# Optimization experiments

Measured on AMD Instinct MI355X. Metric: run time of the kernel, lower is better.

## Reference

```python
import jax, jax.numpy as jnp
from jax import lax
import numpy as np

B, T, V = 2048, 128, 25
H = 512          # num_hidden
NUM_CLASSES = 100


def setup_inputs() -> dict:
    key = jax.random.key(0)
    ks = jax.random.split(key, 7)
    messages = jax.random.normal(ks[0], (B, T, V), dtype=jnp.float32)
    # LSTMCell params (PyTorch layout: weight_ih [4H, V], weight_hh [4H, H], gate order i,f,g,o)
    W_ih = jax.random.normal(ks[1], (4 * H, V), dtype=jnp.float32) * (1.0 / np.sqrt(V))
    W_hh = jax.random.normal(ks[2], (4 * H, H), dtype=jnp.float32) * (1.0 / np.sqrt(H))
    b_ih = jnp.zeros((4 * H,), dtype=jnp.float32)
    # forget-gate bias initialized to 1 (as in initialize_parameters)
    b_hh = jnp.zeros((4 * H,), dtype=jnp.float32).at[H:2 * H].set(1.0)
    W_fc = jax.random.normal(ks[3], (NUM_CLASSES, H), dtype=jnp.float32) * (1.0 / np.sqrt(H))
    b_fc = jnp.zeros((NUM_CLASSES,), dtype=jnp.float32)
    return {"messages": messages, "W_ih": W_ih, "W_hh": W_hh,
            "b_ih": b_ih, "b_hh": b_hh, "W_fc": W_fc, "b_fc": b_fc}


def reference(messages, W_ih, W_hh, b_ih, b_hh, W_fc, b_fc):
    b, t, v = messages.shape
    h_dim = W_hh.shape[1]
    # Batch the input-to-hidden projection across all timesteps up front: [B,T,4H]
    x_proj = jnp.einsum('btv,gv->btg', messages, W_ih) + b_ih + b_hh
    xs = jnp.swapaxes(x_proj, 0, 1)  # [T, B, 4H] for scan over time

    def step(carry, x_g):
        h, c = carry
        gates = x_g + h @ W_hh.T                       # [B, 4H]
        i, f, g, o = jnp.split(gates, 4, axis=-1)      # PyTorch gate order i,f,g,o
        i = jax.nn.sigmoid(i)
        f = jax.nn.sigmoid(f)
        g = jnp.tanh(g)
        o = jax.nn.sigmoid(o)
        c = f * c + i * g
        h = o * jnp.tanh(c)
        return (h, c), None

    init = (jnp.zeros((b, h_dim), dtype=messages.dtype),
            jnp.zeros((b, h_dim), dtype=messages.dtype))
    (h_last, _), _ = lax.scan(step, init, xs)
    return h_last @ W_fc.T + b_fc  # [B, num_classes]
```

## Files before the change

kernel.cpp:

```cpp
#include <hip/hip_runtime.h>

#define BB 2048
#define TT 128
#define VV 25
#define HH 512
#define NC 100

typedef __attribute__((ext_vector_type(8))) _Float16 half8;
typedef __attribute__((ext_vector_type(4))) float f32x4;

__device__ __forceinline__ float fsigmoid(float x) { return 1.0f / (1.0f + __expf(-x)); }
__device__ __forceinline__ float ftanh(float x) {
    float e = __expf(2.0f * x);
    return 1.0f - 2.0f / (e + 1.0f);
}

__global__ __launch_bounds__(256) void prep_whh_t(const float* __restrict__ W,
                                                  _Float16* __restrict__ WT) {
    int i = blockIdx.x * 256 + threadIdx.x;
    int n = i & 2047, kq = i >> 11;
    half8 h8;
    #pragma unroll
    for (int j = 0; j < 8; ++j) h8[j] = (_Float16)W[(size_t)n * HH + kq * 8 + j];
    ((half8*)WT)[(size_t)kq * 2048 + n] = h8;
}

__global__ __launch_bounds__(256) void prep_wih_t(const float* __restrict__ W,
                                                  _Float16* __restrict__ WT) {
    int i = blockIdx.x * 256 + threadIdx.x;
    int n = i & 2047, kq4 = i >> 11;
    half8 h8;
    #pragma unroll
    for (int j = 0; j < 8; ++j) {
        int k = kq4 * 8 + j;
        h8[j] = (k < VV) ? (_Float16)W[(size_t)n * VV + k] : (_Float16)0.0f;
    }
    ((half8*)WT)[(size_t)(64 + kq4) * 2048 + n] = h8;
}

__global__ __launch_bounds__(256, 2) void lstm_step(
    const float* __restrict__ msg, int t,
    const _Float16* __restrict__ WT,
    const float* __restrict__ b_ih, const float* __restrict__ b_hh,
    const _Float16* __restrict__ hin, _Float16* __restrict__ hout,
    float* __restrict__ c)
{
    const int b0 = blockIdx.x * 64;
    const int j0 = blockIdx.y * 32;
    const int tid = threadIdx.x;
    const int lane = tid & 63;
    const int w = tid >> 6;
    const int wm = w & 1, wn = w >> 1;
    const int col = lane & 15, quad = lane >> 4;
    const int jj = j0 + wn * 16 + col;

    __shared__ _Float16 Abuf[2][64][72];

    f32x4 acc[2][4];
    #pragma unroll
    for (int g = 0; g < 4; ++g) {
        float bias = b_ih[g * HH + jj] + b_hh[g * HH + jj];
        f32x4 bv = {bias, bias, bias, bias};
        acc[0][g] = bv;
        acc[1][g] = bv;
    }

    const int arow = tid >> 2, aseg = (tid & 3) << 4;
    const _Float16* aph = hin + (size_t)(b0 + arow) * HH + aseg;

    const half8* WT8 = (const half8*)WT;
    int bidx[4];
    #pragma unroll
    for (int g = 0; g < 4; ++g) bidx[g] = quad * 2048 + g * HH + j0 + wn * 16 + col;

    half8 Bs[2][4];
    half8 ra[2];

    ra[0] = *(const half8*)(aph);
    ra[1] = *(const half8*)(aph + 8);
    #pragma unroll
    for (int g = 0; g < 4; ++g) Bs[0][g] = WT8[bidx[g]];
    *(half8*)&Abuf[0][arow][aseg]     = ra[0];
    *(half8*)&Abuf[0][arow][aseg + 8] = ra[1];
    ra[0] = *(const half8*)(aph + 64);
    ra[1] = *(const half8*)(aph + 72);
    #pragma unroll
    for (int g = 0; g < 4; ++g) Bs[1][g] = WT8[8192 + bidx[g]];
    __syncthreads();

    float xv[8];
    const int xseg = (tid & 3) << 3;

    for (int it = 0; it < 8; ++it) {
        const int buf = it & 1;
        #pragma unroll
        for (int kk = 0; kk < 2; ++kk) {
            const int cchunk = it * 2 + kk;
            const int p = cchunk & 1;
            half8 ahf[2];
            #pragma unroll
            for (int tm = 0; tm < 2; ++tm)
                ahf[tm] = *(const half8*)&Abuf[buf][wm * 32 + tm * 16 + col][kk * 32 + quad * 8];
            #pragma unroll
            for (int tm = 0; tm < 2; ++tm)
                #pragma unroll
                for (int g = 0; g < 4; ++g)
                    acc[tm][g] = __builtin_amdgcn_mfma_f32_16x16x32_f16(ahf[tm], Bs[p][g], acc[tm][g], 0, 0, 0);
            if (cchunk + 2 <= 16) {
                const int ix = (cchunk + 2) * 8192;
                #pragma unroll
                for (int g = 0; g < 4; ++g) Bs[p][g] = WT8[ix + bidx[g]];
            }
        }
        if (it < 7) {
            *(half8*)&Abuf[buf ^ 1][arow][aseg]     = ra[0];
            *(half8*)&Abuf[buf ^ 1][arow][aseg + 8] = ra[1];
            if (it < 6) {
                const int kt = (it + 2) * 64;
                ra[0] = *(const half8*)(aph + kt);
                ra[1] = *(const half8*)(aph + kt + 8);
            } else {
                const size_t mb = ((size_t)(b0 + arow) * TT + t) * VV;
                #pragma unroll
                for (int i = 0; i < 8; ++i) {
                    int k = xseg + i;
                    xv[i] = (k < VV) ? msg[mb + k] : 0.0f;
                }
            }
        } else {
            half8 xh;
            #pragma unroll
            for (int i = 0; i < 8; ++i) xh[i] = (_Float16)xv[i];
            *(half8*)&Abuf[0][arow][xseg] = xh;
        }
        __syncthreads();
    }

    {
        half8 ahf[2];
        #pragma unroll
        for (int tm = 0; tm < 2; ++tm)
            ahf[tm] = *(const half8*)&Abuf[0][wm * 32 + tm * 16 + col][quad * 8];
        #pragma unroll
        for (int tm = 0; tm < 2; ++tm)
            #pragma unroll
            for (int g = 0; g < 4; ++g)
                acc[tm][g] = __builtin_amdgcn_mfma_f32_16x16x32_f16(ahf[tm], Bs[0][g], acc[tm][g], 0, 0, 0);
    }

    #pragma unroll
    for (int tm = 0; tm < 2; ++tm) {
        #pragma unroll
        for (int reg = 0; reg < 4; ++reg) {
            int b = b0 + wm * 32 + tm * 16 + quad * 4 + reg;
            size_t idx = (size_t)b * HH + jj;
            float i_ = fsigmoid(acc[tm][0][reg]);
            float f_ = fsigmoid(acc[tm][1][reg]);
            float g_ = ftanh(acc[tm][2][reg]);
            float o_ = fsigmoid(acc[tm][3][reg]);
            float cn = f_ * c[idx] + i_ * g_;
            c[idx] = cn;
            hout[idx] = (_Float16)(o_ * ftanh(cn));
        }
    }
}

__global__ __launch_bounds__(256) void fc_kernel(
    const _Float16* __restrict__ h, const float* __restrict__ W_fc,
    const float* __restrict__ b_fc, float* __restrict__ out)
{
    __shared__ float hs[4][HH];
    const int b0 = blockIdx.x * 4;
    for (int i = threadIdx.x; i < 4 * HH; i += 256) {
        int r = i >> 9, k = i & 511;
        hs[r][k] = (float)h[(size_t)(b0 + r) * HH + k];
    }
    __syncthreads();
    const int tid = threadIdx.x;
    if (tid < 2 * NC) {
        int r = tid / NC, cls = tid % NC;
        const float4* wv = (const float4*)(W_fc + (size_t)cls * HH);
        const float4* h0 = (const float4*)hs[r];
        const float4* h1 = (const float4*)hs[r + 2];
        float s0 = 0.0f, s1 = 0.0f;
        #pragma unroll 4
        for (int k = 0; k < HH / 4; ++k) {
            float4 ww = wv[k];
            float4 a0 = h0[k], a1 = h1[k];
            s0 += a0.x * ww.x + a0.y * ww.y + a0.z * ww.z + a0.w * ww.w;
            s1 += a1.x * ww.x + a1.y * ww.y + a1.z * ww.z + a1.w * ww.w;
        }
        out[(size_t)(b0 + r) * NC + cls] = s0 + b_fc[cls];
        out[(size_t)(b0 + r + 2) * NC + cls] = s1 + b_fc[cls];
    }
}

extern "C" void kernel_launch(void* const* d_in, const int* in_sizes, int n_in,
                              void* d_out, int out_size, void* d_ws, size_t ws_size,
                              hipStream_t stream) {
    const float* msg  = (const float*)d_in[0];
    const float* W_ih = (const float*)d_in[1];
    const float* W_hh = (const float*)d_in[2];
    const float* b_ih = (const float*)d_in[3];
    const float* b_hh = (const float*)d_in[4];
    const float* W_fc = (const float*)d_in[5];
    const float* b_fc = (const float*)d_in[6];
    float* out = (float*)d_out;

    float*    c  = (float*)d_ws;
    _Float16* h0 = (_Float16*)(c + (size_t)BB * HH);
    _Float16* h1 = h0 + (size_t)BB * HH;
    _Float16* WT = h1 + (size_t)BB * HH;

    hipMemsetAsync(d_ws, 0, (size_t)BB * HH * 4 + (size_t)BB * HH * 2, stream);

    prep_whh_t<<<512, 256, 0, stream>>>(W_hh, WT);
    prep_wih_t<<<32, 256, 0, stream>>>(W_ih, WT);

    _Float16 *hin = h0, *hout = h1;
    for (int t = 0; t < TT; ++t) {
        lstm_step<<<dim3(BB / 64, HH / 32), 256, 0, stream>>>(
            msg, t, WT, b_ih, b_hh, hin, hout, c);
        _Float16* tmp = hin; hin = hout; hout = tmp;
    }
    fc_kernel<<<BB / 4, 256, 0, stream>>>(hin, W_fc, b_fc, out);
}
```

Before: 1.558 ms.

## Load LSTM hidden-state operands directly into registers, drop LDS staging and memset

Replaces the shared-memory double-buffered staging of h with direct per-lane global loads into MFMA operand registers, using a 4-deep register prefetch ring for both A and B fragments and removing all __syncthreads. The t=0 step skips the recurrent matmul and the c read, so the workspace memset goes away. This removes LDS traffic and barrier stalls, but each lane now loads its own h rows with less coalesced access, and register pressure rises, which could hurt occupancy.

```diff
diff --git a/kernel.cpp b/kernel.cpp
--- a/kernel.cpp
+++ b/kernel.cpp
@@ -53,8 +53,7 @@
     const int wm = w & 1, wn = w >> 1;
     const int col = lane & 15, quad = lane >> 4;
     const int jj = j0 + wn * 16 + col;
-
-    __shared__ _Float16 Abuf[2][64][72];
+    const bool first = (t == 0);
 
     f32x4 acc[2][4];
     #pragma unroll
@@ -65,87 +64,90 @@
         acc[1][g] = bv;
     }
 
-    const int arow = tid >> 2, aseg = (tid & 3) << 4;
-    const _Float16* aph = hin + (size_t)(b0 + arow) * HH + aseg;
-
     const half8* WT8 = (const half8*)WT;
     int bidx[4];
     #pragma unroll
-    for (int g = 0; g < 4; ++g) bidx[g] = quad * 2048 + g * HH + j0 + wn * 16 + col;
-
-    half8 Bs[2][4];
-    half8 ra[2];
-
-    ra[0] = *(const half8*)(aph);
-    ra[1] = *(const half8*)(aph + 8);
-    #pragma unroll
-    for (int g = 0; g < 4; ++g) Bs[0][g] = WT8[bidx[g]];
-    *(half8*)&Abuf[0][arow][aseg]     = ra[0];
-    *(half8*)&Abuf[0][arow][aseg + 8] = ra[1];
-    ra[0] = *(const half8*)(aph + 64);
-    ra[1] = *(const half8*)(aph + 72);
-    #pragma unroll
-    for (int g = 0; g < 4; ++g) Bs[1][g] = WT8[8192 + bidx[g]];
-    __syncthreads();
-
-    float xv[8];
-    const int xseg = (tid & 3) << 3;
-
-    for (int it = 0; it < 8; ++it) {
-        const int buf = it & 1;
-        #pragma unroll
-        for (int kk = 0; kk < 2; ++kk) {
-            const int cchunk = it * 2 + kk;
-            const int p = cchunk & 1;
-            half8 ahf[2];
+    for (int g = 0; g < 4; ++g) bidx[g] = quad * 2048 + g * HH + jj;
+
+    const _Float16* aB[2];
+    #pragma unroll
+    for (int tm = 0; tm < 2; ++tm)
+        aB[tm] = hin + (size_t)(b0 + wm * 32 + tm * 16 + col) * HH + quad * 8;
+
+    float xv[2][8];
+    #pragma unroll
+    for (int tm = 0; tm < 2; ++tm) {
+        const size_t mb = ((size_t)(b0 + wm * 32 + tm * 16 + col) * TT + t) * VV;
+        #pragma unroll
+        for (int j = 0; j < 8; ++j) {
+            int k = quad * 8 + j;
+            xv[tm][j] = (k < VV) ? msg[mb + k] : 0.0f;
+        }
+    }
+
+    half8 Ah[4][2];
+    half8 Bs[4][4];
+
+    if (!first) {
+        #pragma unroll
+        for (int pc = 0; pc < 4; ++pc) {
             #pragma unroll
             for (int tm = 0; tm < 2; ++tm)
-                ahf[tm] = *(const half8*)&Abuf[buf][wm * 32 + tm * 16 + col][kk * 32 + quad * 8];
+                Ah[pc][tm] = *(const half8*)(aB[tm] + pc * 32);
+            #pragma unroll
+            for (int g = 0; g < 4; ++g)
+                Bs[pc][g] = WT8[pc * 8192 + bidx[g]];
+        }
+        #pragma unroll
+        for (int cc = 0; cc < 16; ++cc) {
+            const int sl = cc & 3;
             #pragma unroll
             for (int tm = 0; tm < 2; ++tm)
                 #pragma unroll
                 for (int g = 0; g < 4; ++g)
-                    acc[tm][g] = __builtin_amdgcn_mfma_f32_16x16x32_f16(ahf[tm], Bs[p][g], acc[tm][g], 0, 0, 0);
-            if (cchunk + 2 <= 16) {
-                const int ix = (cchunk + 2) * 8192;
-                #pragma unroll
-                for (int g = 0; g < 4; ++g) Bs[p][g] = WT8[ix + bidx[g]];
+                    acc[tm][g] = __builtin_amdgcn_mfma_f32_16x16x32_f16(Ah[sl][tm], Bs[sl][g], acc[tm][g], 0, 0, 0);
+            const int pf = cc + 4;
+            if (pf < 16) {
+                #pragma unroll
+                for (int tm = 0; tm < 2; ++tm)
+                    Ah[sl][tm] = *(const half8*)(aB[tm] + pf * 32);
+                #pragma unroll
+                for (int g = 0; g < 4; ++g)
+                    Bs[sl][g] = WT8[pf * 8192 + bidx[g]];
+            } else if (pf == 16) {
+                #pragma unroll
+                for (int tm = 0; tm < 2; ++tm) {
+                    half8 xh;
+                    #pragma unroll
+                    for (int j = 0; j < 8; ++j) xh[j] = (_Float16)xv[tm][j];
+                    Ah[sl][tm] = xh;
+                }
+                #pragma unroll
+                for (int g = 0; g < 4; ++g)
+                    Bs[sl][g] = WT8[16 * 8192 + bidx[g]];
             }
         }
-        if (it < 7) {
-            *(half8*)&Abuf[buf ^ 1][arow][aseg]     = ra[0];
-            *(half8*)&Abuf[buf ^ 1][arow][aseg + 8] = ra[1];
-            if (it < 6) {
-                const int kt = (it + 2) * 64;
-                ra[0] = *(const half8*)(aph + kt);
-                ra[1] = *(const half8*)(aph + kt + 8);
-            } else {
-                const size_t mb = ((size_t)(b0 + arow) * TT + t) * VV;
-                #pragma unroll
-                for (int i = 0; i < 8; ++i) {
-                    int k = xseg + i;
-                    xv[i] = (k < VV) ? msg[mb + k] : 0.0f;
-                }
-            }
-        } else {
+        #pragma unroll
+        for (int tm = 0; tm < 2; ++tm)
+            #pragma unroll
+            for (int g = 0; g < 4; ++g)
+                acc[tm][g] = __builtin_amdgcn_mfma_f32_16x16x32_f16(Ah[0][tm], Bs[0][g], acc[tm][g], 0, 0, 0);
+    } else {
+        #pragma unroll
+        for (int tm = 0; tm < 2; ++tm) {
             half8 xh;
             #pragma unroll
-            for (int i = 0; i < 8; ++i) xh[i] = (_Float16)xv[i];
-            *(half8*)&Abuf[0][arow][xseg] = xh;
-        }
-        __syncthreads();
-    }
-
-    {
-        half8 ahf[2];
+            for (int j = 0; j < 8; ++j) xh[j] = (_Float16)xv[tm][j];
+            Ah[0][tm] = xh;
+        }
+        #pragma unroll
+        for (int g = 0; g < 4; ++g)
+            Bs[0][g] = WT8[16 * 8192 + bidx[g]];
         #pragma unroll
         for (int tm = 0; tm < 2; ++tm)
-            ahf[tm] = *(const half8*)&Abuf[0][wm * 32 + tm * 16 + col][quad * 8];
-        #pragma unroll
-        for (int tm = 0; tm < 2; ++tm)
             #pragma unroll
             for (int g = 0; g < 4; ++g)
-                acc[tm][g] = __builtin_amdgcn_mfma_f32_16x16x32_f16(ahf[tm], Bs[0][g], acc[tm][g], 0, 0, 0);
+                acc[tm][g] = __builtin_amdgcn_mfma_f32_16x16x32_f16(Ah[0][tm], Bs[0][g], acc[tm][g], 0, 0, 0);
     }
 
     #pragma unroll
@@ -158,7 +160,8 @@
             float f_ = fsigmoid(acc[tm][1][reg]);
             float g_ = ftanh(acc[tm][2][reg]);
             float o_ = fsigmoid(acc[tm][3][reg]);
-            float cn = f_ * c[idx] + i_ * g_;
+            float cn = i_ * g_;
+            if (!first) cn = __builtin_fmaf(f_, c[idx], cn);
             c[idx] = cn;
             hout[idx] = (_Float16)(o_ * ftanh(cn));
         }
@@ -212,8 +215,6 @@
     _Float16* h1 = h0 + (size_t)BB * HH;
     _Float16* WT = h1 + (size_t)BB * HH;
 
-    hipMemsetAsync(d_ws, 0, (size_t)BB * HH * 4 + (size_t)BB * HH * 2, stream);
-
     prep_whh_t<<<512, 256, 0, stream>>>(W_hh, WT);
     prep_wih_t<<<32, 256, 0, stream>>>(W_ih, WT);
 
```

New measurement: 2.690 ms. 1.73x slower.

## Deepen weight prefetch, skip h-GEMM at t=0, load x directly into registers

Applied to the files above, without the earlier changes.

The weight-fragment register pipeline grows from two to four chunks, so global loads of W have more MFMA work to hide behind. Barriers now wait only on LDS counters rather than draining global loads. The message input is loaded straight into MFMA A-fragment registers instead of going through LDS. At t=0 the recurrent GEMM and the c read are skipped because h and c are zero, which also removes the workspace memset. The deeper prefetch raises register pressure, which may lower occupancy under the 2-blocks-per-SM launch bound.

```diff
diff --git a/kernel.cpp b/kernel.cpp
--- a/kernel.cpp
+++ b/kernel.cpp
@@ -13,6 +13,13 @@
 __device__ __forceinline__ float ftanh(float x) {
     float e = __expf(2.0f * x);
     return 1.0f - 2.0f / (e + 1.0f);
+}
+
+__device__ __forceinline__ void bar_nodrain() {
+    asm volatile("s_waitcnt lgkmcnt(0)" ::: "memory");
+    __builtin_amdgcn_sched_barrier(0);
+    __builtin_amdgcn_s_barrier();
+    asm volatile("" ::: "memory");
 }
 
 __global__ __launch_bounds__(256) void prep_whh_t(const float* __restrict__ W,
@@ -53,6 +60,7 @@
     const int wm = w & 1, wn = w >> 1;
     const int col = lane & 15, quad = lane >> 4;
     const int jj = j0 + wn * 16 + col;
+    const bool first = (t == 0);
 
     __shared__ _Float16 Abuf[2][64][72];
 
@@ -71,76 +79,102 @@
     const half8* WT8 = (const half8*)WT;
     int bidx[4];
     #pragma unroll
-    for (int g = 0; g < 4; ++g) bidx[g] = quad * 2048 + g * HH + j0 + wn * 16 + col;
-
-    half8 Bs[2][4];
+    for (int g = 0; g < 4; ++g) bidx[g] = quad * 2048 + g * HH + jj;
+
+    half8 Bs[4][4];
     half8 ra[2];
-
-    ra[0] = *(const half8*)(aph);
-    ra[1] = *(const half8*)(aph + 8);
-    #pragma unroll
-    for (int g = 0; g < 4; ++g) Bs[0][g] = WT8[bidx[g]];
-    *(half8*)&Abuf[0][arow][aseg]     = ra[0];
-    *(half8*)&Abuf[0][arow][aseg + 8] = ra[1];
-    ra[0] = *(const half8*)(aph + 64);
-    ra[1] = *(const half8*)(aph + 72);
-    #pragma unroll
-    for (int g = 0; g < 4; ++g) Bs[1][g] = WT8[8192 + bidx[g]];
-    __syncthreads();
-
-    float xv[8];
-    const int xseg = (tid & 3) << 3;
-
-    for (int it = 0; it < 8; ++it) {
-        const int buf = it & 1;
-        #pragma unroll
-        for (int kk = 0; kk < 2; ++kk) {
-            const int cchunk = it * 2 + kk;
-            const int p = cchunk & 1;
-            half8 ahf[2];
-            #pragma unroll
-            for (int tm = 0; tm < 2; ++tm)
-                ahf[tm] = *(const half8*)&Abuf[buf][wm * 32 + tm * 16 + col][kk * 32 + quad * 8];
-            #pragma unroll
-            for (int tm = 0; tm < 2; ++tm)
+    float xv[2][8];
+
+    if (!first) {
+        ra[0] = *(const half8*)(aph);
+        ra[1] = *(const half8*)(aph + 8);
+        #pragma unroll
+        for (int pc = 0; pc < 4; ++pc)
+            #pragma unroll
+            for (int g = 0; g < 4; ++g) Bs[pc][g] = WT8[pc * 8192 + bidx[g]];
+        *(half8*)&Abuf[0][arow][aseg]     = ra[0];
+        *(half8*)&Abuf[0][arow][aseg + 8] = ra[1];
+        ra[0] = *(const half8*)(aph + 64);
+        ra[1] = *(const half8*)(aph + 72);
+        bar_nodrain();
+
+        #pragma unroll
+        for (int it = 0; it < 8; ++it) {
+            const int buf = it & 1;
+            #pragma unroll
+            for (int kk = 0; kk < 2; ++kk) {
+                const int cc = it * 2 + kk;
+                const int sl = cc & 3;
+                half8 ahf[2];
                 #pragma unroll
-                for (int g = 0; g < 4; ++g)
-                    acc[tm][g] = __builtin_amdgcn_mfma_f32_16x16x32_f16(ahf[tm], Bs[p][g], acc[tm][g], 0, 0, 0);
-            if (cchunk + 2 <= 16) {
-                const int ix = (cchunk + 2) * 8192;
+                for (int tm = 0; tm < 2; ++tm)
+                    ahf[tm] = *(const half8*)&Abuf[buf][wm * 32 + tm * 16 + col][kk * 32 + quad * 8];
                 #pragma unroll
-                for (int g = 0; g < 4; ++g) Bs[p][g] = WT8[ix + bidx[g]];
-            }
-        }
-        if (it < 7) {
-            *(half8*)&Abuf[buf ^ 1][arow][aseg]     = ra[0];
-            *(half8*)&Abuf[buf ^ 1][arow][aseg + 8] = ra[1];
-            if (it < 6) {
-                const int kt = (it + 2) * 64;
-                ra[0] = *(const half8*)(aph + kt);
-                ra[1] = *(const half8*)(aph + kt + 8);
-            } else {
-                const size_t mb = ((size_t)(b0 + arow) * TT + t) * VV;
-                #pragma unroll
-                for (int i = 0; i < 8; ++i) {
-                    int k = xseg + i;
-                    xv[i] = (k < VV) ? msg[mb + k] : 0.0f;
+                for (int tm = 0; tm < 2; ++tm)
+                    #pragma unroll
+                    for (int g = 0; g < 4; ++g)
+                        acc[tm][g] = __builtin_amdgcn_mfma_f32_16x16x32_f16(ahf[tm], Bs[sl][g], acc[tm][g], 0, 0, 0);
+                const int pf = cc + 4;
+                if (pf <= 16) {
+                    #pragma unroll
+                    for (int g = 0; g < 4; ++g) Bs[sl][g] = WT8[pf * 8192 + bidx[g]];
                 }
             }
-        } else {
-            half8 xh;
-            #pragma unroll
-            for (int i = 0; i < 8; ++i) xh[i] = (_Float16)xv[i];
-            *(half8*)&Abuf[0][arow][xseg] = xh;
-        }
-        __syncthreads();
+            if (it < 7) {
+                *(half8*)&Abuf[buf ^ 1][arow][aseg]     = ra[0];
+                *(half8*)&Abuf[buf ^ 1][arow][aseg + 8] = ra[1];
+                if (it < 6) {
+                    const int kt = (it + 2) * 64;
+                    ra[0] = *(const half8*)(aph + kt);
+                    ra[1] = *(const half8*)(aph + kt + 8);
+                } else {
+                    #pragma unroll
+                    for (int tm = 0; tm < 2; ++tm) {
+                        const size_t mb = ((size_t)(b0 + wm * 32 + tm * 16 + col) * TT + t) * VV;
+                        #pragma unroll
+                        for (int j = 0; j < 8; ++j) {
+                            int k = quad * 8 + j;
+                            xv[tm][j] = (k < VV) ? msg[mb + k] : 0.0f;
+                        }
+                    }
+                }
+                bar_nodrain();
+            }
+        }
+    } else {
+        #pragma unroll
+        for (int tm = 0; tm < 2; ++tm) {
+            const size_t mb = ((size_t)(b0 + wm * 32 + tm * 16 + col) * TT + t) * VV;
+            #pragma unroll
+            for (int j = 0; j < 8; ++j) {
+                int k = quad * 8 + j;
+                xv[tm][j] = (k < VV) ? msg[mb + k] : 0.0f;
+            }
+        }
+        #pragma unroll
+        for (int g = 0; g < 4; ++g) Bs[0][g] = WT8[16 * 8192 + bidx[g]];
+    }
+
+    float cv[2][4];
+    if (!first) {
+        #pragma unroll
+        for (int tm = 0; tm < 2; ++tm)
+            #pragma unroll
+            for (int reg = 0; reg < 4; ++reg) {
+                int b = b0 + wm * 32 + tm * 16 + quad * 4 + reg;
+                cv[tm][reg] = c[(size_t)b * HH + jj];
+            }
     }
 
     {
         half8 ahf[2];
         #pragma unroll
-        for (int tm = 0; tm < 2; ++tm)
-            ahf[tm] = *(const half8*)&Abuf[0][wm * 32 + tm * 16 + col][quad * 8];
+        for (int tm = 0; tm < 2; ++tm) {
+            half8 xh;
+            #pragma unroll
+            for (int j = 0; j < 8; ++j) xh[j] = (_Float16)xv[tm][j];
+            ahf[tm] = xh;
+        }
         #pragma unroll
         for (int tm = 0; tm < 2; ++tm)
             #pragma unroll
@@ -158,7 +192,8 @@
             float f_ = fsigmoid(acc[tm][1][reg]);
             float g_ = ftanh(acc[tm][2][reg]);
             float o_ = fsigmoid(acc[tm][3][reg]);
-            float cn = f_ * c[idx] + i_ * g_;
+            float cn = i_ * g_;
+            if (!first) cn = __builtin_fmaf(f_, cv[tm][reg], cn);
             c[idx] = cn;
             hout[idx] = (_Float16)(o_ * ftanh(cn));
         }
@@ -212,8 +247,6 @@
     _Float16* h1 = h0 + (size_t)BB * HH;
     _Float16* WT = h1 + (size_t)BB * HH;
 
-    hipMemsetAsync(d_ws, 0, (size_t)BB * HH * 4 + (size_t)BB * HH * 2, stream);
-
     prep_whh_t<<<512, 256, 0, stream>>>(W_hh, WT);
     prep_wih_t<<<32, 256, 0, stream>>>(W_ih, WT);
 
```

Result: slower. 1.650 ms (+5.9%).
